# Kernel optimization log

Measured on AMD Instinct MI355X. Metric: run time of the kernel, lower is better.

The kernel has to match this reference:

```python
import jax, jax.numpy as jnp
import numpy as np

B, S, L = 32, 512, 64
START, STOP, PAD = 61, 62, 63
NEG = -10000.0


def setup_inputs() -> dict:
    key = jax.random.key(0)
    k1, k2, k3, k4 = jax.random.split(key, 4)
    encoder_scores = jax.random.normal(k1, (B, S, L), dtype=jnp.float32)
    transition = jax.random.normal(k2, (L, L), dtype=jnp.float32)
    # constrained transitions, as in __init__
    transition = (transition.at[:, START].set(NEG)
                            .at[STOP, :].set(NEG)
                            .at[:, PAD].set(NEG)
                            .at[PAD, :].set(NEG))
    word_seq_lens = jax.random.randint(k3, (B,), S // 2, S + 1)  # in [S/2, S]
    tags = jax.random.randint(k4, (B, S), 0, START)  # valid non-special labels
    mask = jnp.arange(S)[None, :] < word_seq_lens[:, None]
    return {"encoder_scores": encoder_scores, "transition": transition,
            "word_seq_lens": word_seq_lens, "tags": tags, "mask": mask}


def reference(encoder_scores, transition, word_seq_lens, tags, mask):
    # all_scores[b,s,i,j] = transition[i,j] + encoder_scores[b,s,j]  (B,S,L,L)
    all_scores = transition[None, None, :, :] + encoder_scores[:, :, None, :]

    # ---- forward algorithm (partition function) ----
    alpha0 = all_scores[:, 0, START, :]  # (B,L)

    def step(a_prev, s_t):  # a_prev (B,L), s_t (B,L,L)
        a = jax.nn.logsumexp(a_prev[:, :, None] + s_t, axis=1)
        return a, a

    _, alphas_rest = jax.lax.scan(step, alpha0,
                                  jnp.swapaxes(all_scores[:, 1:], 0, 1))
    alphas = jnp.concatenate([alpha0[:, None, :],
                              jnp.swapaxes(alphas_rest, 0, 1)], axis=1)  # (B,S,L)
    last_alpha = jnp.take_along_axis(
        alphas, (word_seq_lens - 1)[:, None, None], axis=1)[:, 0, :]  # (B,L)
    last_alpha = last_alpha + transition[:, STOP][None, :]
    unlabeled = jax.nn.logsumexp(last_alpha, axis=1)  # (B,)

    # ---- gold-sequence score ----
    # cur[b,s,i] = all_scores[b,s,i,tags[b,s]]
    cur = jnp.take_along_axis(all_scores, tags[:, :, None, None], axis=3)[..., 0]  # (B,S,L)
    mid = jnp.take_along_axis(cur[:, 1:, :], tags[:, :-1, None], axis=2)[..., 0]  # (B,S-1)
    begin = cur[:, 0, START]  # (B,)
    end_ids = jnp.take_along_axis(tags, (word_seq_lens - 1)[:, None], axis=1)[:, 0]
    end_sc = transition[end_ids, STOP]  # (B,)
    labeled = begin + end_sc + jnp.sum(mid * mask[:, 1:].astype(mid.dtype), axis=1)
    return unlabeled, labeled
```

## Files before the change

### kernel.cpp

```cpp
#include <hip/hip_runtime.h>

#define BB 32
#define SS 512
#define LL 64
#define TSTART 61
#define TSTOP 62
#define NSEG 16
#define SEGLEN 32
#define QPAD 68

typedef short short8 __attribute__((ext_vector_type(8)));
typedef float floatx4 __attribute__((ext_vector_type(4)));

union S8 { int i[4]; short8 v; };

__device__ inline unsigned bf16_rne(float x) {
    unsigned u = __float_as_uint(x);
    u += 0x7fffu + ((u >> 16) & 1u);
    return u >> 16;
}
__device__ inline int pack_bf16(float a, float b) {
    return (int)(bf16_rne(a) | (bf16_rne(b) << 16));
}

__global__ __launch_bounds__(64) void crf_seg_kernel(
    const float* __restrict__ enc, const float* __restrict__ Tr,
    const int* __restrict__ lens, const int* __restrict__ tags,
    float* __restrict__ wsQ, float* __restrict__ wsS,
    float* __restrict__ out)
{
    const int blk = blockIdx.x;
    if (blk >= BB * NSEG * 4) {
        const int b = blk - BB * NSEG * 4;
        const int tid = threadIdx.x;
        const int len = lens[b];
        const int* tg = tags + b * SS;
        const float* eb = enc + b * (SS * LL);
        float acc = 0.f;
        for (int t = 1 + tid; t < len; t += 64) {
            int curt = tg[t], prevt = tg[t - 1];
            acc += Tr[prevt * LL + curt] + eb[t * LL + curt];
        }
        #pragma unroll
        for (int off = 32; off; off >>= 1) acc += __shfl_xor(acc, off);
        if (tid == 0) {
            int t0 = tg[0], te = tg[len - 1];
            acc += Tr[TSTART * LL + t0] + eb[t0];
            acc += Tr[te * LL + TSTOP];
            out[BB + b] = acc;
        }
        return;
    }

    const int lane = threadIdx.x;
    const int b = blk >> 6;
    const int s = (blk >> 2) & 15;
    const int g = blk & 3;
    const int len = lens[b];
    const int q = lane >> 4;
    const int lcol = lane & 15;
    const float* eb = enc + b * (SS * LL);
    const int tlo = SEGLEN * s + 1;
    const int Teff = min(max(len - tlo, 0), SEGLEN);

    float* qdst = wsQ + (size_t)(b * NSEG + s) * 4096;

    if (Teff <= 0) {
        #pragma unroll
        for (int u = 0; u < 4; ++u) {
            int r0 = 16 * q + 4 * u;
            float4 v;
            v.x = (r0 + 0 == 16 * g + lcol) ? 1.f : 0.f;
            v.y = (r0 + 1 == 16 * g + lcol) ? 1.f : 0.f;
            v.z = (r0 + 2 == 16 * g + lcol) ? 1.f : 0.f;
            v.w = (r0 + 3 == 16 * g + lcol) ? 1.f : 0.f;
            *(float4*)(qdst + (16 * g + lcol) * 64 + r0) = v;
        }
        if (lane == 0) wsS[(b * NSEG + s) * 4 + g] = 0.f;
        return;
    }

    __shared__ __align__(16) float QT[16 * QPAD];
    __shared__ __align__(16) float W32[32 * 64];

    short8 Afr[4][2];
    #pragma unroll
    for (int mt = 0; mt < 4; ++mt)
        #pragma unroll
        for (int c2 = 0; c2 < 2; ++c2) {
            float av[8];
            #pragma unroll
            for (int idx = 0; idx < 8; ++idx) {
                int kk = 32 * c2 + 8 * q + idx;
                int mm = 16 * mt + lcol;
                av[idx] = __expf(Tr[kk * LL + mm]) * 0.0078125f;
            }
            S8 u;
            #pragma unroll
            for (int w2 = 0; w2 < 4; ++w2) u.i[w2] = pack_bf16(av[2 * w2], av[2 * w2 + 1]);
            Afr[mt][c2] = u.v;
        }

    {
        const float* trow = Tr + (16 * g + lcol) * LL;
        #pragma unroll
        for (int u = 0; u < 4; ++u) {
            float4 tv = *(const float4*)(trow + 16 * q + 4 * u);
            float4 ev;
            ev.x = __expf(tv.x) * 0.0078125f;
            ev.y = __expf(tv.y) * 0.0078125f;
            ev.z = __expf(tv.z) * 0.0078125f;
            ev.w = __expf(tv.w) * 0.0078125f;
            *(float4*)(QT + lcol * QPAD + 16 * q + 4 * u) = ev;
        }
    }

    float lg = 0.0f;
    float ecur[8], enxt[8];
    #pragma unroll
    for (int k = 0; k < 8; ++k) ecur[k] = eb[min(tlo + k, SS - 1) * LL + lane];
    #pragma unroll
    for (int k = 0; k < 8; ++k) enxt[k] = eb[min(tlo + 8 + k, SS - 1) * LL + lane];

    for (int cc = 0; cc < 4; ++cc) {
        #pragma unroll
        for (int k = 0; k < 8; ++k) W32[(8 * cc + k) * 64 + lane] = __expf(ecur[k]);
        float epre[8];
        #pragma unroll
        for (int k = 0; k < 8; ++k) epre[k] = eb[min(tlo + 8 * (cc + 2) + k, SS - 1) * LL + lane];

        #pragma unroll
        for (int k = 0; k < 8; ++k) {
            const int i = 8 * cc + k + 2;
            if (i <= Teff) {
                const int wloc = 8 * cc + k;
                float4 qv[2][2], wv[2][2];
                #pragma unroll
                for (int c2 = 0; c2 < 2; ++c2)
                    #pragma unroll
                    for (int h = 0; h < 2; ++h) {
                        qv[c2][h] = *(const float4*)(QT + lcol * QPAD + 32 * c2 + 8 * q + 4 * h);
                        wv[c2][h] = *(const float4*)(W32 + wloc * 64 + 32 * c2 + 8 * q + 4 * h);
                    }
                short8 Bfr[2];
                #pragma unroll
                for (int c2 = 0; c2 < 2; ++c2) {
                    float bv[8];
                    bv[0] = qv[c2][0].x * wv[c2][0].x;  bv[1] = qv[c2][0].y * wv[c2][0].y;
                    bv[2] = qv[c2][0].z * wv[c2][0].z;  bv[3] = qv[c2][0].w * wv[c2][0].w;
                    bv[4] = qv[c2][1].x * wv[c2][1].x;  bv[5] = qv[c2][1].y * wv[c2][1].y;
                    bv[6] = qv[c2][1].z * wv[c2][1].z;  bv[7] = qv[c2][1].w * wv[c2][1].w;
                    S8 u;
                    #pragma unroll
                    for (int w2 = 0; w2 < 4; ++w2)
                        u.i[w2] = pack_bf16(bv[2 * w2], bv[2 * w2 + 1]);
                    Bfr[c2] = u.v;
                }
                float ov[4][4];
                #pragma unroll
                for (int mt = 0; mt < 4; ++mt) {
                    floatx4 z = {0.f, 0.f, 0.f, 0.f};
                    z = __builtin_amdgcn_mfma_f32_16x16x32_bf16(Afr[mt][0], Bfr[0], z, 0, 0, 0);
                    z = __builtin_amdgcn_mfma_f32_16x16x32_bf16(Afr[mt][1], Bfr[1], z, 0, 0, 0);
                    ov[mt][0] = z[0]; ov[mt][1] = z[1]; ov[mt][2] = z[2]; ov[mt][3] = z[3];
                }
                if (k == 7) {
                    float mx = ov[0][0];
                    #pragma unroll
                    for (int mt = 0; mt < 4; ++mt)
                        #pragma unroll
                        for (int r = 0; r < 4; ++r) mx = fmaxf(mx, ov[mt][r]);
                    #pragma unroll
                    for (int off = 32; off; off >>= 1) mx = fmaxf(mx, __shfl_xor(mx, off));
                    lg += __logf(mx);
                    float rmx = 1.0f / mx;
                    #pragma unroll
                    for (int mt = 0; mt < 4; ++mt)
                        #pragma unroll
                        for (int r = 0; r < 4; ++r) ov[mt][r] *= rmx;
                }
                #pragma unroll
                for (int mt = 0; mt < 4; ++mt) {
                    float4 sv = make_float4(ov[mt][0], ov[mt][1], ov[mt][2], ov[mt][3]);
                    *(float4*)(QT + lcol * QPAD + 16 * mt + 4 * q) = sv;
                }
            }
        }
        #pragma unroll
        for (int k = 0; k < 8; ++k) { ecur[k] = enxt[k]; enxt[k] = epre[k]; }
    }

    const float* wl = W32 + (Teff - 1) * 64;
    #pragma unroll
    for (int u = 0; u < 4; ++u) {
        int r0 = 16 * q + 4 * u;
        float4 mv = *(const float4*)(QT + lcol * QPAD + r0);
        float4 wv = *(const float4*)(wl + r0);
        float4 o = make_float4(mv.x * wv.x, mv.y * wv.y, mv.z * wv.z, mv.w * wv.w);
        *(float4*)(qdst + (16 * g + lcol) * 64 + r0) = o;
    }
    if (lane == 0) wsS[(b * NSEG + s) * 4 + g] = lg;
}

__global__ __launch_bounds__(64) void crf_combine_kernel(
    const float* __restrict__ enc, const float* __restrict__ Tr,
    const int* __restrict__ lens,
    const float* __restrict__ wsQ, const float* __restrict__ wsS,
    float* __restrict__ out)
{
    const int b = blockIdx.x;
    const int j = threadIdx.x;
    const int len = lens[b];
    const float* qb = wsQ + (size_t)b * NSEG * 4096;

    float alpha0 = Tr[TSTART * LL + j] + enc[b * (SS * LL) + j];
    float m = alpha0;
    #pragma unroll
    for (int off = 32; off; off >>= 1) m = fmaxf(m, __shfl_xor(m, off));
    float a = __expf(alpha0 - m);
    float logscale = m;

    float myscale = wsS[b * (NSEG * 4) + j];

    float A[64], Bv[64];
    #pragma unroll
    for (int c = 0; c < 64; ++c) A[c] = qb[c * 64 + j];

    auto step = [&](int s, float (&cur)[64]) {
        float l0 = __shfl(myscale, 4 * s + 0);
        float l1 = __shfl(myscale, 4 * s + 1);
        float l2 = __shfl(myscale, 4 * s + 2);
        float l3 = __shfl(myscale, 4 * s + 3);
        float lmax = fmaxf(fmaxf(l0, l1), fmaxf(l2, l3));
        int grp = j >> 4;
        float lgg = (grp == 0) ? l0 : (grp == 1) ? l1 : (grp == 2) ? l2 : l3;
        float at = a * __expf(lgg - lmax);
        int ai = __float_as_int(at);
        float s0 = 0.f, s1 = 0.f, s2 = 0.f, s3 = 0.f;
        #pragma unroll
        for (int c = 0; c < 16; ++c) {
            s0 = fmaf(__int_as_float(__builtin_amdgcn_readlane(ai, 4 * c + 0)), cur[4 * c + 0], s0);
            s1 = fmaf(__int_as_float(__builtin_amdgcn_readlane(ai, 4 * c + 1)), cur[4 * c + 1], s1);
            s2 = fmaf(__int_as_float(__builtin_amdgcn_readlane(ai, 4 * c + 2)), cur[4 * c + 2], s2);
            s3 = fmaf(__int_as_float(__builtin_amdgcn_readlane(ai, 4 * c + 3)), cur[4 * c + 3], s3);
        }
        float an = ((s0 + s1) + (s2 + s3));
        float mx = an;
        #pragma unroll
        for (int off = 32; off; off >>= 1) mx = fmaxf(mx, __shfl_xor(mx, off));
        a = an * (1.0f / mx);
        logscale += lmax + __logf(mx);
    };

    for (int s = 0; s < 16; s += 2) {
        const float* q1 = qb + (size_t)min(s + 1, NSEG - 1) * 4096;
        #pragma unroll
        for (int c = 0; c < 64; ++c) Bv[c] = q1[c * 64 + j];
        step(s, A);
        const float* q2 = qb + (size_t)min(s + 2, NSEG - 1) * 4096;
        #pragma unroll
        for (int c = 0; c < 64; ++c) A[c] = q2[c * 64 + j];
        step(s + 1, Bv);
    }

    float f = a * __expf(Tr[j * LL + TSTOP]);
    float ssum = f;
    #pragma unroll
    for (int off = 32; off; off >>= 1) ssum += __shfl_xor(ssum, off);
    if (j == 0) {
        const float LN2x7 = 7.0f * 0.69314718055994530942f;
        out[b] = logscale + (float)(len - 1) * LN2x7 + __logf(ssum);
    }
}

__global__ __launch_bounds__(256) void crf_kernel_fb(
    const float* __restrict__ enc, const float* __restrict__ Tr,
    const int* __restrict__ lens, const int* __restrict__ tags,
    float* __restrict__ out)
{
    if (blockIdx.x < BB) {
        const int tid = threadIdx.x;
        if (tid >= 64) return;
        const int b = blockIdx.x;
        const int j = tid;
        const int len = lens[b];
        const float* eb = enc + b * (SS * LL);
        float Ecol[LL];
        #pragma unroll
        for (int i = 0; i < LL; ++i) Ecol[i] = __expf(Tr[i * LL + j]) * 0.0078125f;
        float alpha0 = Tr[TSTART * LL + j] + eb[j];
        float m = alpha0;
        #pragma unroll
        for (int off = 32; off; off >>= 1) m = fmaxf(m, __shfl_xor(m, off));
        float a = __expf(alpha0 - m);
        float logscale = m;
        float ecur[4], enext[4];
        #pragma unroll
        for (int k = 0; k < 4; ++k) ecur[k] = eb[k * LL + j];
        #pragma unroll
        for (int k = 0; k < 4; ++k) enext[k] = eb[(4 + k) * LL + j];
        const int nchunk = (len + 3) >> 2;
        for (int c = 0; c < nchunk; ++c) {
            const int cpre = (c + 2 < 128) ? (c + 2) : 127;
            float efar[4];
            #pragma unroll
            for (int k = 0; k < 4; ++k) efar[k] = eb[(4 * cpre + k) * LL + j];
            #pragma unroll
            for (int k = 0; k < 4; ++k) {
                const int t = 4 * c + k;
                if (t >= 1 && t < len) {
                    const float w = __expf(ecur[k]);
                    const int ai = __float_as_int(a);
                    float s0 = 0.f, s1 = 0.f, s2 = 0.f, s3 = 0.f;
                    #pragma unroll
                    for (int qq = 0; qq < 16; ++qq) {
                        s0 = fmaf(__int_as_float(__builtin_amdgcn_readlane(ai, 4 * qq + 0)), Ecol[4 * qq + 0], s0);
                        s1 = fmaf(__int_as_float(__builtin_amdgcn_readlane(ai, 4 * qq + 1)), Ecol[4 * qq + 1], s1);
                        s2 = fmaf(__int_as_float(__builtin_amdgcn_readlane(ai, 4 * qq + 2)), Ecol[4 * qq + 2], s2);
                        s3 = fmaf(__int_as_float(__builtin_amdgcn_readlane(ai, 4 * qq + 3)), Ecol[4 * qq + 3], s3);
                    }
                    a = ((s0 + s1) + (s2 + s3)) * w;
                    if ((t & 7) == 7) {
                        float mm = a;
                        #pragma unroll
                        for (int off = 32; off; off >>= 1) mm = fmaxf(mm, __shfl_xor(mm, off));
                        logscale += __logf(mm);
                        a = a * (1.0f / mm);
                    }
                }
            }
            #pragma unroll
            for (int k = 0; k < 4; ++k) { ecur[k] = enext[k]; enext[k] = efar[k]; }
        }
        float f = a * __expf(Tr[j * LL + TSTOP]);
        float ssum = f;
        #pragma unroll
        for (int off = 32; off; off >>= 1) ssum += __shfl_xor(ssum, off);
        if (j == 0) {
            const float LN2x7 = 7.0f * 0.69314718055994530942f;
            out[b] = logscale + (float)(len - 1) * LN2x7 + __logf(ssum);
        }
    } else {
        const int b = blockIdx.x - BB;
        const int tid = threadIdx.x;
        const int len = lens[b];
        const int* tg = tags + b * SS;
        const float* eb = enc + b * (SS * LL);
        float acc = 0.f;
        for (int t = 1 + tid; t < len; t += 256) {
            int curt = tg[t], prevt = tg[t - 1];
            acc += Tr[prevt * LL + curt] + eb[t * LL + curt];
        }
        #pragma unroll
        for (int off = 32; off; off >>= 1) acc += __shfl_xor(acc, off);
        __shared__ float red[4];
        if ((tid & 63) == 0) red[tid >> 6] = acc;
        __syncthreads();
        if (tid == 0) {
            float tot = (red[0] + red[1]) + (red[2] + red[3]);
            int t0 = tg[0], te = tg[len - 1];
            tot += Tr[TSTART * LL + t0] + eb[t0];
            tot += Tr[te * LL + TSTOP];
            out[BB + b] = tot;
        }
    }
}

extern "C" void kernel_launch(void* const* d_in, const int* in_sizes, int n_in,
                              void* d_out, int out_size, void* d_ws, size_t ws_size,
                              hipStream_t stream) {
    const float* enc  = (const float*)d_in[0];
    const float* Tr   = (const float*)d_in[1];
    const int*   lens = (const int*)d_in[2];
    const int*   tags = (const int*)d_in[3];
    float* out = (float*)d_out;

    const size_t needQ = (size_t)BB * NSEG * 4096 * sizeof(float);
    const size_t needS = (size_t)BB * NSEG * 4 * sizeof(float);
    if (ws_size >= needQ + needS) {
        float* wsQ = (float*)d_ws;
        float* wsS = (float*)((char*)d_ws + needQ);
        crf_seg_kernel<<<BB * NSEG * 4 + BB, 64, 0, stream>>>(enc, Tr, lens, tags, wsQ, wsS, out);
        crf_combine_kernel<<<BB, 64, 0, stream>>>(enc, Tr, lens, wsQ, wsS, out);
    } else {
        crf_kernel_fb<<<2 * BB, 256, 0, stream>>>(enc, Tr, lens, tags, out);
    }
}
```

Measured before the change: 99.81 us.

## Transpose workspace Q layout so combine kernel loads rows with float4

The segment kernel now writes each thread's Q column contiguously (row = lane, columns 16g..16g+15), so the combine kernel can read its 64 coefficients with 16 float4 loads instead of 64 strided scalar loads. The block-to-(batch, segment, group) mapping is also changed to interleave 8 batches across neighbouring block indices, which may balance work across CUs. The trade-off is strided scalar LDS reads from QT in the segment kernel and partial-row 64-byte global writes.

```diff
diff --git a/kernel.cpp b/kernel.cpp
--- a/kernel.cpp
+++ b/kernel.cpp
@@ -53,9 +53,12 @@
     }
 
     const int lane = threadIdx.x;
-    const int b = blk >> 6;
-    const int s = (blk >> 2) & 15;
-    const int g = blk & 3;
+    const int xr = blk & 7;
+    const int pk = blk >> 3;
+    const int b = xr + 8 * (pk >> 6);
+    const int rem = pk & 63;
+    const int s = rem >> 2;
+    const int g = rem & 3;
     const int len = lens[b];
     const int q = lane >> 4;
     const int lcol = lane & 15;
@@ -67,14 +70,14 @@
 
     if (Teff <= 0) {
         #pragma unroll
-        for (int u = 0; u < 4; ++u) {
-            int r0 = 16 * q + 4 * u;
+        for (int c4 = 0; c4 < 4; ++c4) {
+            int c0 = 16 * g + 4 * c4;
             float4 v;
-            v.x = (r0 + 0 == 16 * g + lcol) ? 1.f : 0.f;
-            v.y = (r0 + 1 == 16 * g + lcol) ? 1.f : 0.f;
-            v.z = (r0 + 2 == 16 * g + lcol) ? 1.f : 0.f;
-            v.w = (r0 + 3 == 16 * g + lcol) ? 1.f : 0.f;
-            *(float4*)(qdst + (16 * g + lcol) * 64 + r0) = v;
+            v.x = (c0 + 0 == lane) ? 1.f : 0.f;
+            v.y = (c0 + 1 == lane) ? 1.f : 0.f;
+            v.z = (c0 + 2 == lane) ? 1.f : 0.f;
+            v.w = (c0 + 3 == lane) ? 1.f : 0.f;
+            *(float4*)(qdst + lane * 64 + c0) = v;
         }
         if (lane == 0) wsS[(b * NSEG + s) * 4 + g] = 0.f;
         return;
@@ -190,14 +193,17 @@
         for (int k = 0; k < 8; ++k) { ecur[k] = enxt[k]; enxt[k] = epre[k]; }
     }
 
-    const float* wl = W32 + (Teff - 1) * 64;
-    #pragma unroll
-    for (int u = 0; u < 4; ++u) {
-        int r0 = 16 * q + 4 * u;
-        float4 mv = *(const float4*)(QT + lcol * QPAD + r0);
-        float4 wv = *(const float4*)(wl + r0);
-        float4 o = make_float4(mv.x * wv.x, mv.y * wv.y, mv.z * wv.z, mv.w * wv.w);
-        *(float4*)(qdst + (16 * g + lcol) * 64 + r0) = o;
+    {
+        const float wj = W32[(Teff - 1) * 64 + lane];
+        #pragma unroll
+        for (int c4 = 0; c4 < 4; ++c4) {
+            float4 o;
+            o.x = QT[(4 * c4 + 0) * QPAD + lane] * wj;
+            o.y = QT[(4 * c4 + 1) * QPAD + lane] * wj;
+            o.z = QT[(4 * c4 + 2) * QPAD + lane] * wj;
+            o.w = QT[(4 * c4 + 3) * QPAD + lane] * wj;
+            *(float4*)(qdst + lane * 64 + 16 * g + 4 * c4) = o;
+        }
     }
     if (lane == 0) wsS[(b * NSEG + s) * 4 + g] = lg;
 }
@@ -224,7 +230,10 @@
 
     float A[64], Bv[64];
     #pragma unroll
-    for (int c = 0; c < 64; ++c) A[c] = qb[c * 64 + j];
+    for (int i = 0; i < 16; ++i) {
+        float4 t = *(const float4*)(qb + j * 64 + 4 * i);
+        A[4 * i + 0] = t.x; A[4 * i + 1] = t.y; A[4 * i + 2] = t.z; A[4 * i + 3] = t.w;
+    }
 
     auto step = [&](int s, float (&cur)[64]) {
         float l0 = __shfl(myscale, 4 * s + 0);
@@ -255,11 +264,17 @@
     for (int s = 0; s < 16; s += 2) {
         const float* q1 = qb + (size_t)min(s + 1, NSEG - 1) * 4096;
         #pragma unroll
-        for (int c = 0; c < 64; ++c) Bv[c] = q1[c * 64 + j];
+        for (int i = 0; i < 16; ++i) {
+            float4 t = *(const float4*)(q1 + j * 64 + 4 * i);
+            Bv[4 * i + 0] = t.x; Bv[4 * i + 1] = t.y; Bv[4 * i + 2] = t.z; Bv[4 * i + 3] = t.w;
+        }
         step(s, A);
         const float* q2 = qb + (size_t)min(s + 2, NSEG - 1) * 4096;
         #pragma unroll
-        for (int c = 0; c < 64; ++c) A[c] = q2[c * 64 + j];
+        for (int i = 0; i < 16; ++i) {
+            float4 t = *(const float4*)(q2 + j * 64 + 4 * i);
+            A[4 * i + 0] = t.x; A[4 * i + 1] = t.y; A[4 * i + 2] = t.z; A[4 * i + 3] = t.w;
+        }
         step(s + 1, Bv);
     }
 
```

New measurement: 98.33 us. No clear change (-1.5%).
